# Optimization experiments

Measured on AMD Instinct MI355X. Metric: run time of the kernel, lower is better.

The kernel has to match this reference:

```python
import jax, jax.numpy as jnp
import numpy as np

C = 1.0        # curvature parameter (manifold curvature -1/C)
EPS = 1e-7


def expmap0_space(v, k):
    # v: [..., ds] spatial tangent vector at the hyperboloid origin (time comp 0)
    # returns ambient point [..., ds+1] = (sqrt(k)cosh(|v|/sqrt(k)), sqrt(k)sinh(|v|/sqrt(k)) v/|v|)
    sk = jnp.sqrt(k)
    n = jnp.maximum(jnp.linalg.norm(v, axis=-1, keepdims=True), EPS)
    t = sk * jnp.cosh(n / sk)
    s = sk * jnp.sinh(n / sk) * (v / n)
    return jnp.concatenate([t, s], axis=-1)


def logmap0_space(p, k):
    # p: [..., ds+1] hyperboloid point -> spatial tangent [..., ds] at origin
    sk = jnp.sqrt(k)
    t, s = p[..., :1], p[..., 1:]
    ns = jnp.maximum(jnp.linalg.norm(s, axis=-1, keepdims=True), EPS)
    d = sk * jnp.arccosh(jnp.maximum(t / sk, 1.0 + EPS))
    return d * (s / ns)


def setup_inputs() -> dict:
    key = jax.random.key(0)
    N, DS, E = 50000, 127, 800000
    ks = jax.random.split(key, 8)
    x = jax.random.normal(ks[0], (N, DS), dtype=jnp.float32) * 0.1
    edge_src = jax.random.randint(ks[1], (E,), 0, N)
    edge_dst = jax.random.randint(ks[2], (E,), 0, N)
    edge_weight = jax.random.uniform(ks[3], (E,), dtype=jnp.float32) / 16.0  # ~1/deg norm
    sc = 1.0 / np.sqrt(DS)
    W1 = jax.random.normal(ks[4], (DS, DS), dtype=jnp.float32) * sc
    b1 = jnp.zeros((DS,), dtype=jnp.float32)
    W2 = jax.random.normal(ks[5], (DS, DS), dtype=jnp.float32) * sc
    b2 = jnp.zeros((DS,), dtype=jnp.float32)
    return {"x": x, "W1": W1, "b1": b1, "W2": W2, "b2": b2,
            "edge_src": edge_src, "edge_dst": edge_dst, "edge_weight": edge_weight}


def reference(x, W1, b1, W2, b2, edge_src, edge_dst, edge_weight):
    N = x.shape[0]
    # encode(): cat zero time column + expmap0 onto hyperboloid
    p = expmap0_space(x, C)                 # [N, ds+1]
    h = logmap0_space(p, C)                 # tangent features at origin [N, ds]
    for (W, b) in ((W1, b1), (W2, b2)):
        # hyperbolic linear in tangent space
        z = h @ W + b                       # [N, ds]
        # adjacency-based neighbor aggregation (sparse spmm via edge list)
        msg = edge_weight[:, None] * z[edge_src]          # [E, ds] irregular gather
        agg = jax.ops.segment_sum(msg, edge_dst, num_segments=N)
        # activation + skip connection, back onto the manifold between layers
        h = jax.nn.relu(agg) + h
        h = logmap0_space(expmap0_space(h, C), C)
    return expmap0_space(h, C)              # [N, ds+1] on hyperboloid
```

## Files before the change

kernel.cpp:

```cpp
#include <hip/hip_runtime.h>

#define EPS 1e-7f
#define DS 127
#define DP 128
#define NBMAX 512
#define CAP 4096
#define CH 2048
#define PADB ((DP * DP + DP + 255) / 256)

typedef short bf16x8 __attribute__((ext_vector_type(8)));
typedef float f32x4  __attribute__((ext_vector_type(4)));
typedef float f32x2  __attribute__((ext_vector_type(2)));

__device__ __forceinline__ float wave_sum(float v) {
#pragma unroll
    for (int off = 32; off > 0; off >>= 1)
        v += __shfl_xor(v, off, 64);
    return v;
}

__device__ __forceinline__ int wave_sum_i(int v) {
#pragma unroll
    for (int off = 32; off > 0; off >>= 1)
        v += __shfl_xor(v, off, 64);
    return v;
}

__device__ __forceinline__ unsigned short f2bf(float f) {
    unsigned u = __float_as_uint(f);
    unsigned r = (u + 0x7FFFu + ((u >> 16) & 1u)) >> 16;
    return (unsigned short)r;
}

__device__ __forceinline__ unsigned pack_bf2(float a, float b) {
    return (unsigned)f2bf(a) | ((unsigned)f2bf(b) << 16);
}

__device__ __forceinline__ unsigned char f2fp8(float v) {
    return (unsigned char)(__builtin_amdgcn_cvt_pk_fp8_f32(v, v, 0, false) & 0xFF);
}

__device__ __forceinline__ float logexp_scale(float n2) {
    float nrm = sqrtf(n2);
    return (nrm >= 4.472136e-4f) ? 1.0f : (4.472136e-4f / fmaxf(nrm, EPS));
}

__device__ __forceinline__ void sinhcosh(float n, float& sh, float& ch) {
    float e  = __expf(n);
    float em = __expf(-n);
    sh = 0.5f * (e - em);
    ch = 0.5f * (e + em);
}

__device__ __forceinline__ void padT_dev(int pb, int tid,
        const float* __restrict__ W, const float* __restrict__ b,
        unsigned short* __restrict__ Wt, float* __restrict__ bp) {
    int i = pb * 256 + tid;
    if (i < DP * DP) {
        int n = i >> 7, k = i & (DP - 1);
        Wt[i] = (k < DS && n < DS) ? f2bf(W[k * DS + n]) : (unsigned short)0;
    } else if (i < DP * DP + DP) {
        int j = i - DP * DP;
        bp[j] = (j < DS) ? b[j] : 0.f;
    }
}

__device__ __forceinline__ void f_first_dev(int fbid, int tid,
        const float* __restrict__ x, unsigned* __restrict__ hbu, int N) {
    int gw   = fbid * 4 + (tid >> 6);
    int lane = tid & 63;
    if (gw >= N) return;

    const float* row = x + (size_t)gw * DS;
    float x0 = row[2 * lane];
    float x1 = (lane < 63) ? row[2 * lane + 1] : 0.f;

    float scale = logexp_scale(wave_sum(x0 * x0 + x1 * x1));
    hbu[(size_t)gw * (DP / 2) + lane] = pack_bf2(scale * x0,
                                                 (lane < 63) ? scale * x1 : 0.f);
}

__device__ void binA_dev(int abid, int tid,
        const int* __restrict__ es, const int* __restrict__ ed,
        const float* __restrict__ ew,
        int* __restrict__ gcnt, unsigned* __restrict__ stg_pk,
        unsigned char* __restrict__ stg_r, int E) {
    __shared__ int  lcnt[NBMAX];
    __shared__ int  loff[NBMAX];
    __shared__ int  gbase[NBMAX];
    __shared__ unsigned       lst_pk[CH];
    __shared__ unsigned short lst_d[CH];

    int lane = tid & 63;
    int base = abid * CH;
    int cnt  = min(CH, E - base);

    for (int b = tid; b < NBMAX; b += 256) lcnt[b] = 0;
    __syncthreads();

    unsigned pk[CH / 256];
    int      rd[CH / 256];
#pragma unroll
    for (int k = 0; k < CH / 256; k++) {
        int i = base + k * 256 + tid;
        if (i < E) {
            int d = ed[i];
            rd[k] = d;
            pk[k] = ((unsigned)f2bf(ew[i]) << 16) | (unsigned)es[i];
            atomicAdd(&lcnt[d >> 7], 1);
        } else {
            rd[k] = -1;
        }
    }
    __syncthreads();

    if (tid < 64) {
        int carry = 0;
        for (int c = 0; c < NBMAX; c += 64) {
            int v = lcnt[c + lane];
            int inc = v;
#pragma unroll
            for (int off = 1; off < 64; off <<= 1) {
                int t = __shfl_up(inc, off, 64);
                if (lane >= off) inc += t;
            }
            loff[c + lane] = carry + inc - v;
            carry += __shfl(inc, 63, 64);
        }
    }
    __syncthreads();
    for (int b = tid; b < NBMAX; b += 256) lcnt[b] = 0;
    __syncthreads();

#pragma unroll
    for (int k = 0; k < CH / 256; k++) {
        if (rd[k] >= 0) {
            int b = rd[k] >> 7;
            int slot = loff[b] + atomicAdd(&lcnt[b], 1);
            lst_pk[slot] = pk[k];
            lst_d[slot]  = (unsigned short)rd[k];
        }
    }
    __syncthreads();

    for (int b = tid; b < NBMAX; b += 256) {
        int c = lcnt[b];
        gbase[b] = c ? atomicAdd(&gcnt[b], c) : 0;
    }
    __syncthreads();

    for (int s = tid; s < cnt; s += 256) {
        unsigned p = lst_pk[s];
        int d = lst_d[s];
        int b = d >> 7;
        int idx = gbase[b] + (s - loff[b]);
        if (idx >= CAP) idx = CAP - 1;
        stg_pk[(size_t)b * CAP + idx] = p;
        stg_r [(size_t)b * CAP + idx] = (unsigned char)(d & 127);
    }
}

__global__ __launch_bounds__(256) void mega1(
        const float* __restrict__ x, unsigned* __restrict__ hbu, int N,
        const float* __restrict__ W1, const float* __restrict__ b1,
        unsigned short* __restrict__ Wt1, float* __restrict__ bp1,
        const float* __restrict__ W2, const float* __restrict__ b2,
        unsigned short* __restrict__ Wt2, float* __restrict__ bp2,
        const int* __restrict__ es, const int* __restrict__ ed,
        const float* __restrict__ ew,
        int* __restrict__ gcnt, unsigned* __restrict__ stg_pk,
        unsigned char* __restrict__ stg_r, int E, int nA) {
    int bid = blockIdx.x;
    int tid = threadIdx.x;

    if (bid < nA) {
        binA_dev(bid, tid, es, ed, ew, gcnt, stg_pk, stg_r, E);
        return;
    }
    bid -= nA;

    if (bid < 2 * PADB) {
        int layer = (bid >= PADB);
        int pb    = bid - layer * PADB;
        padT_dev(pb, tid, layer ? W2 : W1, layer ? b2 : b1,
                 layer ? Wt2 : Wt1, layer ? bp2 : bp1);
        return;
    }
    bid -= 2 * PADB;

    f_first_dev(bid, tid, x, hbu, N);
}

__device__ void binB_dev(int b, int tid,
        const unsigned* __restrict__ stg_pk, const unsigned char* __restrict__ stg_r,
        const int* __restrict__ gcnt,
        int* __restrict__ row_start, unsigned* __restrict__ epk,
        int N, int E) {
    __shared__ int rcnt[128];
    __shared__ int roff[128];
    __shared__ int sh_bb;

    int lane = tid & 63;
    int wave = tid >> 6;
    int cnt  = min(gcnt[b], CAP);
    const unsigned*      in_pk = stg_pk + (size_t)b * CAP;
    const unsigned char* in_r  = stg_r  + (size_t)b * CAP;

    if (tid < 128) rcnt[tid] = 0;
    if (b == 0 && tid == 0) row_start[N] = E;
    __syncthreads();

    if (wave == 3) {
        int acc = 0;
        for (int c = lane; c < b; c += 64) acc += min(gcnt[c], CAP);
        acc = wave_sum_i(acc);
        if (lane == 0) sh_bb = acc;
    } else {
        for (int i = tid; i < cnt; i += 192)
            atomicAdd(&rcnt[in_r[i]], 1);
    }
    __syncthreads();
    int bb = sh_bb;

    if (tid < 64) {
        int carry = 0;
        for (int c = 0; c < 128; c += 64) {
            int v = rcnt[c + lane];
            int inc = v;
#pragma unroll
            for (int off = 1; off < 64; off <<= 1) {
                int t = __shfl_up(inc, off, 64);
                if (lane >= off) inc += t;
            }
            roff[c + lane] = carry + inc - v;
            carry += __shfl(inc, 63, 64);
        }
    }
    __syncthreads();

    if (tid < 128) {
        int row = b * 128 + tid;
        if (row < N) row_start[row] = bb + roff[tid];
        rcnt[tid] = 0;
    }
    __syncthreads();

    for (int i = tid; i < cnt; i += 256) {
        int r = in_r[i];
        int pos = atomicAdd(&rcnt[r], 1);
        epk[bb + roff[r] + pos] = in_pk[i];
    }
}

#define BM 64
__device__ void gemm_dev(int gbid, int tid,
        const unsigned short* __restrict__ hb,
        const unsigned short* __restrict__ Wt,
        const float* __restrict__ bp,
        unsigned char* __restrict__ z8, int N) {
    int wave = tid >> 6;
    int lane = tid & 63;
    int m    = lane & 15;
    int quad = lane >> 4;
    int r0   = gbid * BM + wave * 16;

    f32x4 acc[8];
#pragma unroll
    for (int t = 0; t < 8; t++) acc[t] = (f32x4){0.f, 0.f, 0.f, 0.f};

    const bf16x8* arow = (const bf16x8*)(hb + (size_t)(r0 + m) * DP);
#pragma unroll
    for (int kq = 0; kq < 4; kq++) {
        bf16x8 a = arow[kq * 4 + quad];
#pragma unroll
        for (int nt = 0; nt < 8; nt++) {
            bf16x8 bfr = ((const bf16x8*)(Wt + (size_t)(nt * 16 + m) * DP))[kq * 4 + quad];
            acc[nt] = __builtin_amdgcn_mfma_f32_16x16x32_bf16(a, bfr, acc[nt], 0, 0, 0);
        }
    }

#pragma unroll
    for (int nt = 0; nt < 8; nt++) {
        float bias = bp[nt * 16 + m];
#pragma unroll
        for (int reg = 0; reg < 4; reg++) {
            int row = r0 + quad * 4 + reg;
            if (row < N)
                z8[(size_t)row * DP + nt * 16 + m] = f2fp8(acc[nt][reg] + bias);
        }
    }
}

__global__ __launch_bounds__(256) void mega2(
        const unsigned* __restrict__ stg_pk, const unsigned char* __restrict__ stg_r,
        const int* __restrict__ gcnt,
        int* __restrict__ row_start, unsigned* __restrict__ epk,
        const unsigned short* __restrict__ hb,
        const unsigned short* __restrict__ Wt,
        const float* __restrict__ bp,
        unsigned char* __restrict__ z8, int N, int E, int nB) {
    int bid = blockIdx.x;
    int tid = threadIdx.x;
    if (bid < nB) {
        binB_dev(bid, tid, stg_pk, stg_r, gcnt, row_start, epk, N, E);
        return;
    }
    gemm_dev(bid - nB, tid, hb, Wt, bp, z8, N);
}

#define GATHER(K)                                                             \
    {                                                                         \
        unsigned pks[K], us[K];                                               \
        _Pragma("unroll")                                                     \
        for (int i = 0; i < K; i++) pks[i] = epk[e + i];                      \
        _Pragma("unroll")                                                     \
        for (int i = 0; i < K; i++)                                           \
            us[i] = *(const unsigned short*)(zc + (((pks[i] & 0xFFFFu) << 7) + lane2)); \
        _Pragma("unroll")                                                     \
        for (int i = 0; i < K; i++) {                                         \
            float wf = __uint_as_float(pks[i] & 0xFFFF0000u);                 \
            f32x2 zv = __builtin_amdgcn_cvt_pk_f32_fp8(us[i], false);         \
            a0 = fmaf(wf, zv.x, a0);                                          \
            a1 = fmaf(wf, zv.y, a1);                                          \
        }                                                                     \
    }

#define GATHER_TAIL(K)                                                        \
    {                                                                         \
        unsigned pks[K], us[K];                                               \
        _Pragma("unroll")                                                     \
        for (int i = 0; i < K; i++) {                                         \
            int ii = e + i;                                                   \
            int ic = (ii < end) ? ii : (end - 1);                             \
            unsigned p = epk[ic];                                             \
            pks[i] = (ii < end) ? p : 0u;                                     \
        }                                                                     \
        _Pragma("unroll")                                                     \
        for (int i = 0; i < K; i++)                                           \
            us[i] = *(const unsigned short*)(zc + (((pks[i] & 0xFFFFu) << 7) + lane2)); \
        _Pragma("unroll")                                                     \
        for (int i = 0; i < K; i++) {                                         \
            float wf = __uint_as_float(pks[i] & 0xFFFF0000u);                 \
            f32x2 zv = __builtin_amdgcn_cvt_pk_f32_fp8(us[i], false);         \
            a0 = fmaf(wf, zv.x, a0);                                          \
            a1 = fmaf(wf, zv.y, a1);                                          \
        }                                                                     \
    }

template <bool LAST>
__global__ __launch_bounds__(256) void agg_f_tpl(
                          const unsigned char* __restrict__ zc,
                          const unsigned* __restrict__ hbu_in,
                          const int* __restrict__ row_start,
                          const unsigned* __restrict__ epk,
                          unsigned* __restrict__ hbu_out,
                          float* __restrict__ out, int N) {
    int gw   = (int)((blockIdx.x * blockDim.x + threadIdx.x) >> 6);
    int lane = threadIdx.x & 63;
    if (gw >= N) return;
    gw = __builtin_amdgcn_readfirstlane(gw);
    int lane2 = lane << 1;

    int beg = row_start[gw], end = row_start[gw + 1];
    float a0 = 0.f, a1 = 0.f;

    int e = beg;
    for (; e + 16 <= end; e += 16) GATHER(16)
    if (e < end) GATHER_TAIL(16)

    unsigned hu = hbu_in[(size_t)gw * (DP / 2) + lane];
    float x0 = __uint_as_float(hu << 16) + fmaxf(a0, 0.f);
    float x1 = (lane < 63) ? __uint_as_float(hu & 0xFFFF0000u) + fmaxf(a1, 0.f)
                           : 0.f;

    float n2 = wave_sum(x0 * x0 + x1 * x1);
    float scale = logexp_scale(n2);
    float y0 = scale * x0;
    float y1 = (lane < 63) ? scale * x1 : 0.f;

    if (!LAST) {
        hbu_out[(size_t)gw * (DP / 2) + lane] = pack_bf2(y0, y1);
    } else {
        float n2y = scale * scale * n2;
        float ny  = fmaxf(sqrtf(n2y), EPS);
        float shy, chy;
        sinhcosh(ny, shy, chy);
        float sc  = shy / ny;
        float* orow = out + (size_t)gw * DP;
        if (lane == 0) orow[0] = chy;
        orow[1 + 2 * lane] = sc * y0;
        if (lane < 63) orow[2 + 2 * lane] = sc * y1;
    }
}

extern "C" void kernel_launch(void* const* d_in, const int* in_sizes, int n_in,
                              void* d_out, int out_size, void* d_ws, size_t ws_size,
                              hipStream_t stream) {
    const float* x  = (const float*)d_in[0];
    const float* W1 = (const float*)d_in[1];
    const float* b1 = (const float*)d_in[2];
    const float* W2 = (const float*)d_in[3];
    const float* b2 = (const float*)d_in[4];
    const int*   es = (const int*)d_in[5];
    const int*   ed = (const int*)d_in[6];
    const float* ew = (const float*)d_in[7];

    const int N  = in_sizes[0] / DS;
    const int E  = in_sizes[5];
    const int NR = (N + BM - 1) / BM * BM;
    const int NB = (N + 127) >> 7;

    unsigned short* hb  = (unsigned short*)d_ws;
    unsigned char*  z8  = (unsigned char*)(hb + (size_t)NR * DP);
    unsigned short* Wt1 = (unsigned short*)(z8 + (size_t)N * DP);
    unsigned short* Wt2 = Wt1 + DP * DP;
    float* bp1          = (float*)(Wt2 + DP * DP);
    float* bp2          = bp1 + DP;
    unsigned* epk       = (unsigned*)(bp2 + DP);
    int*   row_start    = (int*)(epk + E);
    int*   gcnt         = row_start + N + 1;
    unsigned* stg_pk    = (unsigned*)(gcnt + NBMAX);
    unsigned char* stg_r = (unsigned char*)(stg_pk + (size_t)NBMAX * CAP);

    unsigned* hbu = (unsigned*)hb;

    const int fBlocks    = (N * 64 + 255) / 256;
    const int gemmBlocks = (N + BM - 1) / BM;
    const int binABlocks = (E + CH - 1) / CH;

    hipMemsetAsync(gcnt, 0, NBMAX * sizeof(int), stream);

    mega1<<<binABlocks + 2 * PADB + fBlocks, 256, 0, stream>>>(
        x, hbu, N, W1, b1, Wt1, bp1, W2, b2, Wt2, bp2,
        es, ed, ew, gcnt, stg_pk, stg_r, E, binABlocks);

    mega2<<<NB + gemmBlocks, 256, 0, stream>>>(
        stg_pk, stg_r, gcnt, row_start, epk, hb, Wt1, bp1, z8, N, E, NB);

    agg_f_tpl<false><<<fBlocks, 256, 0, stream>>>(z8, hbu, row_start, epk,
                                                  hbu, nullptr, N);

    mega2<<<gemmBlocks, 256, 0, stream>>>(
        stg_pk, stg_r, gcnt, row_start, epk, hb, Wt2, bp2, z8, N, E, 0);

    agg_f_tpl<true><<<fBlocks, 256, 0, stream>>>(z8, hbu, row_start, epk,
                                                 nullptr, (float*)d_out, N);
}
```

Baseline: 220.0 us.

## Fuse first encode into layer-1 GEMM, process two rows per wave in aggregation

The initial expmap/logmap encode of x moves out of the first mega kernel and into the layer-1 GEMM blocks. Each block normalises its 64 rows, stages them as bf16 in LDS and feeds MFMA directly from there, which removes a global round trip of h before the first GEMM. The aggregation kernel now handles two destination rows per wave, and the row histogram in binB reads uchar4. The second-layer GEMM becomes a standalone kernel. The fused GEMM adds 16 KB of LDS and more register pressure in a kernel that shares blocks with binB, and handling two rows serially per wave may reduce parallelism in the gather.

```diff
diff --git a/kernel.cpp b/kernel.cpp
--- a/kernel.cpp
+++ b/kernel.cpp
@@ -7,6 +7,7 @@
 #define CAP 4096
 #define CH 2048
 #define PADB ((DP * DP + DP + 255) / 256)
+#define BM 64
 
 typedef short bf16x8 __attribute__((ext_vector_type(8)));
 typedef float f32x4  __attribute__((ext_vector_type(4)));
@@ -65,21 +66,6 @@
     }
 }
 
-__device__ __forceinline__ void f_first_dev(int fbid, int tid,
-        const float* __restrict__ x, unsigned* __restrict__ hbu, int N) {
-    int gw   = fbid * 4 + (tid >> 6);
-    int lane = tid & 63;
-    if (gw >= N) return;
-
-    const float* row = x + (size_t)gw * DS;
-    float x0 = row[2 * lane];
-    float x1 = (lane < 63) ? row[2 * lane + 1] : 0.f;
-
-    float scale = logexp_scale(wave_sum(x0 * x0 + x1 * x1));
-    hbu[(size_t)gw * (DP / 2) + lane] = pack_bf2(scale * x0,
-                                                 (lane < 63) ? scale * x1 : 0.f);
-}
-
 __device__ void binA_dev(int abid, int tid,
         const int* __restrict__ es, const int* __restrict__ ed,
         const float* __restrict__ ew,
@@ -160,37 +146,6 @@
     }
 }
 
-__global__ __launch_bounds__(256) void mega1(
-        const float* __restrict__ x, unsigned* __restrict__ hbu, int N,
-        const float* __restrict__ W1, const float* __restrict__ b1,
-        unsigned short* __restrict__ Wt1, float* __restrict__ bp1,
-        const float* __restrict__ W2, const float* __restrict__ b2,
-        unsigned short* __restrict__ Wt2, float* __restrict__ bp2,
-        const int* __restrict__ es, const int* __restrict__ ed,
-        const float* __restrict__ ew,
-        int* __restrict__ gcnt, unsigned* __restrict__ stg_pk,
-        unsigned char* __restrict__ stg_r, int E, int nA) {
-    int bid = blockIdx.x;
-    int tid = threadIdx.x;
-
-    if (bid < nA) {
-        binA_dev(bid, tid, es, ed, ew, gcnt, stg_pk, stg_r, E);
-        return;
-    }
-    bid -= nA;
-
-    if (bid < 2 * PADB) {
-        int layer = (bid >= PADB);
-        int pb    = bid - layer * PADB;
-        padT_dev(pb, tid, layer ? W2 : W1, layer ? b2 : b1,
-                 layer ? Wt2 : Wt1, layer ? bp2 : bp1);
-        return;
-    }
-    bid -= 2 * PADB;
-
-    f_first_dev(bid, tid, x, hbu, N);
-}
-
 __device__ void binB_dev(int b, int tid,
         const unsigned* __restrict__ stg_pk, const unsigned char* __restrict__ stg_r,
         const int* __restrict__ gcnt,
@@ -216,7 +171,16 @@
         acc = wave_sum_i(acc);
         if (lane == 0) sh_bb = acc;
     } else {
-        for (int i = tid; i < cnt; i += 192)
+        int n4 = cnt >> 2;
+        const uchar4* in_r4 = (const uchar4*)in_r;
+        for (int i = tid; i < n4; i += 192) {
+            uchar4 v = in_r4[i];
+            atomicAdd(&rcnt[v.x], 1);
+            atomicAdd(&rcnt[v.y], 1);
+            atomicAdd(&rcnt[v.z], 1);
+            atomicAdd(&rcnt[v.w], 1);
+        }
+        for (int i = (n4 << 2) + tid; i < cnt; i += 192)
             atomicAdd(&rcnt[in_r[i]], 1);
     }
     __syncthreads();
@@ -252,52 +216,101 @@
     }
 }
 
-#define BM 64
-__device__ void gemm_dev(int gbid, int tid,
-        const unsigned short* __restrict__ hb,
-        const unsigned short* __restrict__ Wt,
-        const float* __restrict__ bp,
+__global__ __launch_bounds__(256) void k1_kernel(
+        const int* __restrict__ es, const int* __restrict__ ed,
+        const float* __restrict__ ew,
+        int* __restrict__ gcnt, unsigned* __restrict__ stg_pk,
+        unsigned char* __restrict__ stg_r, int E,
+        const float* __restrict__ W1, const float* __restrict__ b1,
+        unsigned short* __restrict__ Wt1, float* __restrict__ bp1,
+        const float* __restrict__ W2, const float* __restrict__ b2,
+        unsigned short* __restrict__ Wt2, float* __restrict__ bp2, int nA) {
+    int bid = blockIdx.x;
+    int tid = threadIdx.x;
+    if (bid < nA) {
+        binA_dev(bid, tid, es, ed, ew, gcnt, stg_pk, stg_r, E);
+        return;
+    }
+    bid -= nA;
+    int layer = (bid >= PADB);
+    int pb    = bid - layer * PADB;
+    padT_dev(pb, tid, layer ? W2 : W1, layer ? b2 : b1,
+             layer ? Wt2 : Wt1, layer ? bp2 : bp1);
+}
+
+__device__ void fgemm_dev(int gbid, int tid,
+        const float* __restrict__ x, unsigned* __restrict__ hbu,
+        const unsigned short* __restrict__ Wt, const float* __restrict__ bp,
         unsigned char* __restrict__ z8, int N) {
+    __shared__ unsigned sha[64 * 64];
+
     int wave = tid >> 6;
     int lane = tid & 63;
+    int r0   = gbid * BM;
+
+    f32x2 xv[16];
+#pragma unroll
+    for (int r = 0; r < 16; r++) {
+        int row = r0 + wave * 16 + r;
+        if (row < N) {
+            const float* rp = x + (size_t)row * DS;
+            xv[r].x = rp[2 * lane];
+            xv[r].y = (lane < 63) ? rp[2 * lane + 1] : 0.f;
+        } else {
+            xv[r].x = 0.f; xv[r].y = 0.f;
+        }
+    }
+#pragma unroll
+    for (int r = 0; r < 16; r++) {
+        int lr  = wave * 16 + r;
+        int row = r0 + lr;
+        float s = logexp_scale(wave_sum(xv[r].x * xv[r].x + xv[r].y * xv[r].y));
+        unsigned pk = pack_bf2(s * xv[r].x, (lane < 63) ? s * xv[r].y : 0.f);
+        sha[lr * 64 + lane] = pk;
+        if (row < N) hbu[(size_t)row * (DP / 2) + lane] = pk;
+    }
+
     int m    = lane & 15;
     int quad = lane >> 4;
-    int r0   = gbid * BM + wave * 16;
 
     f32x4 acc[8];
 #pragma unroll
     for (int t = 0; t < 8; t++) acc[t] = (f32x4){0.f, 0.f, 0.f, 0.f};
 
-    const bf16x8* arow = (const bf16x8*)(hb + (size_t)(r0 + m) * DP);
+    const unsigned* shrow = sha + (size_t)(wave * 16 + m) * 64;
+    bf16x8 a[4];
+#pragma unroll
+    for (int kq = 0; kq < 4; kq++)
+        a[kq] = *(const bf16x8*)(shrow + kq * 16 + quad * 4);
+
 #pragma unroll
     for (int kq = 0; kq < 4; kq++) {
-        bf16x8 a = arow[kq * 4 + quad];
 #pragma unroll
         for (int nt = 0; nt < 8; nt++) {
             bf16x8 bfr = ((const bf16x8*)(Wt + (size_t)(nt * 16 + m) * DP))[kq * 4 + quad];
-            acc[nt] = __builtin_amdgcn_mfma_f32_16x16x32_bf16(a, bfr, acc[nt], 0, 0, 0);
-        }
-    }
-
+            acc[nt] = __builtin_amdgcn_mfma_f32_16x16x32_bf16(a[kq], bfr, acc[nt], 0, 0, 0);
+        }
+    }
+
+    int rw0 = r0 + wave * 16;
 #pragma unroll
     for (int nt = 0; nt < 8; nt++) {
         float bias = bp[nt * 16 + m];
 #pragma unroll
         for (int reg = 0; reg < 4; reg++) {
-            int row = r0 + quad * 4 + reg;
+            int row = rw0 + quad * 4 + reg;
             if (row < N)
                 z8[(size_t)row * DP + nt * 16 + m] = f2fp8(acc[nt][reg] + bias);
         }
     }
 }
 
-__global__ __launch_bounds__(256) void mega2(
+__global__ __launch_bounds__(256) void k2_kernel(
         const unsigned* __restrict__ stg_pk, const unsigned char* __restrict__ stg_r,
         const int* __restrict__ gcnt,
         int* __restrict__ row_start, unsigned* __restrict__ epk,
-        const unsigned short* __restrict__ hb,
-        const unsigned short* __restrict__ Wt,
-        const float* __restrict__ bp,
+        const float* __restrict__ x, unsigned* __restrict__ hbu,
+        const unsigned short* __restrict__ Wt, const float* __restrict__ bp,
         unsigned char* __restrict__ z8, int N, int E, int nB) {
     int bid = blockIdx.x;
     int tid = threadIdx.x;
@@ -305,47 +318,90 @@
         binB_dev(bid, tid, stg_pk, stg_r, gcnt, row_start, epk, N, E);
         return;
     }
-    gemm_dev(bid - nB, tid, hb, Wt, bp, z8, N);
-}
-
-#define GATHER(K)                                                             \
-    {                                                                         \
-        unsigned pks[K], us[K];                                               \
-        _Pragma("unroll")                                                     \
-        for (int i = 0; i < K; i++) pks[i] = epk[e + i];                      \
-        _Pragma("unroll")                                                     \
-        for (int i = 0; i < K; i++)                                           \
-            us[i] = *(const unsigned short*)(zc + (((pks[i] & 0xFFFFu) << 7) + lane2)); \
-        _Pragma("unroll")                                                     \
-        for (int i = 0; i < K; i++) {                                         \
-            float wf = __uint_as_float(pks[i] & 0xFFFF0000u);                 \
-            f32x2 zv = __builtin_amdgcn_cvt_pk_f32_fp8(us[i], false);         \
-            a0 = fmaf(wf, zv.x, a0);                                          \
-            a1 = fmaf(wf, zv.y, a1);                                          \
-        }                                                                     \
-    }
-
-#define GATHER_TAIL(K)                                                        \
-    {                                                                         \
-        unsigned pks[K], us[K];                                               \
-        _Pragma("unroll")                                                     \
-        for (int i = 0; i < K; i++) {                                         \
-            int ii = e + i;                                                   \
-            int ic = (ii < end) ? ii : (end - 1);                             \
-            unsigned p = epk[ic];                                             \
-            pks[i] = (ii < end) ? p : 0u;                                     \
-        }                                                                     \
-        _Pragma("unroll")                                                     \
-        for (int i = 0; i < K; i++)                                           \
-            us[i] = *(const unsigned short*)(zc + (((pks[i] & 0xFFFFu) << 7) + lane2)); \
-        _Pragma("unroll")                                                     \
-        for (int i = 0; i < K; i++) {                                         \
-            float wf = __uint_as_float(pks[i] & 0xFFFF0000u);                 \
-            f32x2 zv = __builtin_amdgcn_cvt_pk_f32_fp8(us[i], false);         \
-            a0 = fmaf(wf, zv.x, a0);                                          \
-            a1 = fmaf(wf, zv.y, a1);                                          \
-        }                                                                     \
-    }
+    fgemm_dev(bid - nB, tid, x, hbu, Wt, bp, z8, N);
+}
+
+__global__ __launch_bounds__(256) void gemm_kernel(
+        const unsigned short* __restrict__ hb,
+        const unsigned short* __restrict__ Wt,
+        const float* __restrict__ bp,
+        unsigned char* __restrict__ z8, int N) {
+    int wave = threadIdx.x >> 6;
+    int lane = threadIdx.x & 63;
+    int m    = lane & 15;
+    int quad = lane >> 4;
+    int r0   = blockIdx.x * BM + wave * 16;
+
+    f32x4 acc[8];
+#pragma unroll
+    for (int t = 0; t < 8; t++) acc[t] = (f32x4){0.f, 0.f, 0.f, 0.f};
+
+    const bf16x8* arow = (const bf16x8*)(hb + (size_t)(r0 + m) * DP);
+    bf16x8 a[4];
+#pragma unroll
+    for (int kq = 0; kq < 4; kq++) a[kq] = arow[kq * 4 + quad];
+
+#pragma unroll
+    for (int kq = 0; kq < 4; kq++) {
+#pragma unroll
+        for (int nt = 0; nt < 8; nt++) {
+            bf16x8 bfr = ((const bf16x8*)(Wt + (size_t)(nt * 16 + m) * DP))[kq * 4 + quad];
+            acc[nt] = __builtin_amdgcn_mfma_f32_16x16x32_bf16(a[kq], bfr, acc[nt], 0, 0, 0);
+        }
+    }
+
+#pragma unroll
+    for (int nt = 0; nt < 8; nt++) {
+        float bias = bp[nt * 16 + m];
+#pragma unroll
+        for (int reg = 0; reg < 4; reg++) {
+            int row = r0 + quad * 4 + reg;
+            if (row < N)
+                z8[(size_t)row * DP + nt * 16 + m] = f2fp8(acc[nt][reg] + bias);
+        }
+    }
+}
+
+__device__ __forceinline__ void gather16(const unsigned char* __restrict__ zc,
+        const unsigned* __restrict__ epk, int e, int lane2,
+        float& a0, float& a1) {
+    unsigned pks[16], us[16];
+#pragma unroll
+    for (int i = 0; i < 16; i++) pks[i] = epk[e + i];
+#pragma unroll
+    for (int i = 0; i < 16; i++)
+        us[i] = *(const unsigned short*)(zc + (((pks[i] & 0xFFFFu) << 7) + lane2));
+#pragma unroll
+    for (int i = 0; i < 16; i++) {
+        float wf = __uint_as_float(pks[i] & 0xFFFF0000u);
+        f32x2 zv = __builtin_amdgcn_cvt_pk_f32_fp8(us[i], false);
+        a0 = fmaf(wf, zv.x, a0);
+        a1 = fmaf(wf, zv.y, a1);
+    }
+}
+
+__device__ __forceinline__ void gather_tail16(const unsigned char* __restrict__ zc,
+        const unsigned* __restrict__ epk, int e, int end, int lane2,
+        float& a0, float& a1) {
+    unsigned pks[16], us[16];
+#pragma unroll
+    for (int i = 0; i < 16; i++) {
+        int ii = e + i;
+        int ic = (ii < end) ? ii : (end - 1);
+        unsigned p = epk[ic];
+        pks[i] = (ii < end) ? p : 0u;
+    }
+#pragma unroll
+    for (int i = 0; i < 16; i++)
+        us[i] = *(const unsigned short*)(zc + (((pks[i] & 0xFFFFu) << 7) + lane2));
+#pragma unroll
+    for (int i = 0; i < 16; i++) {
+        float wf = __uint_as_float(pks[i] & 0xFFFF0000u);
+        f32x2 zv = __builtin_amdgcn_cvt_pk_f32_fp8(us[i], false);
+        a0 = fmaf(wf, zv.x, a0);
+        a1 = fmaf(wf, zv.y, a1);
+    }
+}
 
 template <bool LAST>
 __global__ __launch_bounds__(256) void agg_f_tpl(
@@ -355,41 +411,58 @@
                           const unsigned* __restrict__ epk,
                           unsigned* __restrict__ hbu_out,
                           float* __restrict__ out, int N) {
-    int gw   = (int)((blockIdx.x * blockDim.x + threadIdx.x) >> 6);
+    int wid  = (int)((blockIdx.x * blockDim.x + threadIdx.x) >> 6);
     int lane = threadIdx.x & 63;
-    if (gw >= N) return;
-    gw = __builtin_amdgcn_readfirstlane(gw);
+    int gw0  = wid * 2;
+    if (gw0 >= N) return;
+    gw0 = __builtin_amdgcn_readfirstlane(gw0);
     int lane2 = lane << 1;
-
-    int beg = row_start[gw], end = row_start[gw + 1];
-    float a0 = 0.f, a1 = 0.f;
-
-    int e = beg;
-    for (; e + 16 <= end; e += 16) GATHER(16)
-    if (e < end) GATHER_TAIL(16)
-
-    unsigned hu = hbu_in[(size_t)gw * (DP / 2) + lane];
-    float x0 = __uint_as_float(hu << 16) + fmaxf(a0, 0.f);
-    float x1 = (lane < 63) ? __uint_as_float(hu & 0xFFFF0000u) + fmaxf(a1, 0.f)
-                           : 0.f;
-
-    float n2 = wave_sum(x0 * x0 + x1 * x1);
-    float scale = logexp_scale(n2);
-    float y0 = scale * x0;
-    float y1 = (lane < 63) ? scale * x1 : 0.f;
-
-    if (!LAST) {
-        hbu_out[(size_t)gw * (DP / 2) + lane] = pack_bf2(y0, y1);
-    } else {
-        float n2y = scale * scale * n2;
-        float ny  = fmaxf(sqrtf(n2y), EPS);
-        float shy, chy;
-        sinhcosh(ny, shy, chy);
-        float sc  = shy / ny;
-        float* orow = out + (size_t)gw * DP;
-        if (lane == 0) orow[0] = chy;
-        orow[1 + 2 * lane] = sc * y0;
-        if (lane < 63) orow[2 + 2 * lane] = sc * y1;
+    bool has1 = (gw0 + 1 < N);
+
+    int rs0 = row_start[gw0];
+    int rs1 = row_start[gw0 + 1];
+    int rs2 = has1 ? row_start[gw0 + 2] : rs1;
+    unsigned hu0 = hbu_in[(size_t)gw0 * (DP / 2) + lane];
+    unsigned hu1 = has1 ? hbu_in[(size_t)(gw0 + 1) * (DP / 2) + lane] : 0u;
+
+    int begs[2] = {rs0, rs1};
+    int ends[2] = {rs1, rs2};
+    float a0[2] = {0.f, 0.f}, a1[2] = {0.f, 0.f};
+
+#pragma unroll
+    for (int r = 0; r < 2; r++) {
+        int e = begs[r], end = ends[r];
+        for (; e + 16 <= end; e += 16) gather16(zc, epk, e, lane2, a0[r], a1[r]);
+        if (e < end) gather_tail16(zc, epk, e, end, lane2, a0[r], a1[r]);
+    }
+
+    unsigned hus[2] = {hu0, hu1};
+#pragma unroll
+    for (int r = 0; r < 2; r++) {
+        if (r == 1 && !has1) break;
+        int gw = gw0 + r;
+        float x0 = __uint_as_float(hus[r] << 16) + fmaxf(a0[r], 0.f);
+        float x1 = (lane < 63) ? __uint_as_float(hus[r] & 0xFFFF0000u) + fmaxf(a1[r], 0.f)
+                               : 0.f;
+
+        float n2 = wave_sum(x0 * x0 + x1 * x1);
+        float scale = logexp_scale(n2);
+        float y0 = scale * x0;
+        float y1 = (lane < 63) ? scale * x1 : 0.f;
+
+        if (!LAST) {
+            hbu_out[(size_t)gw * (DP / 2) + lane] = pack_bf2(y0, y1);
+        } else {
+            float n2y = scale * scale * n2;
+            float ny  = fmaxf(sqrtf(n2y), EPS);
+            float shy, chy;
+            sinhcosh(ny, shy, chy);
+            float sc  = shy / ny;
+            float* orow = out + (size_t)gw * DP;
+            if (lane == 0) orow[0] = chy;
+            orow[1 + 2 * lane] = sc * y0;
+            if (lane < 63) orow[2 + 2 * lane] = sc * y1;
+        }
     }
 }
 
@@ -424,25 +497,26 @@
 
     unsigned* hbu = (unsigned*)hb;
 
-    const int fBlocks    = (N * 64 + 255) / 256;
     const int gemmBlocks = (N + BM - 1) / BM;
     const int binABlocks = (E + CH - 1) / CH;
+    const int aggWaves   = (N + 1) / 2;
+    const int aggBlocks  = (aggWaves + 3) / 4;
 
     hipMemsetAsync(gcnt, 0, NBMAX * sizeof(int), stream);
 
-    mega1<<<binABlocks + 2 * PADB + fBlocks, 256, 0, stream>>>(
-        x, hbu, N, W1, b1, Wt1, bp1, W2, b2, Wt2, bp2,
-        es, ed, ew, gcnt, stg_pk, stg_r, E, binABlocks);
-
-    mega2<<<NB + gemmBlocks, 256, 0, stream>>>(
-        stg_pk, stg_r, gcnt, row_start, epk, hb, Wt1, bp1, z8, N, E, NB);
-
-    agg_f_tpl<false><<<fBlocks, 256, 0, stream>>>(z8, hbu, row_start, epk,
-                                                  hbu, nullptr, N);
-
-    mega2<<<gemmBlocks, 256, 0, stream>>>(
-        stg_pk, stg_r, gcnt, row_start, epk, hb, Wt2, bp2, z8, N, E, 0);
-
-    agg_f_tpl<true><<<fBlocks, 256, 0, stream>>>(z8, hbu, row_start, epk,
-                                                 nullptr, (float*)d_out, N);
-}
+    k1_kernel<<<binABlocks + 2 * PADB, 256, 0, stream>>>(
+        es, ed, ew, gcnt, stg_pk, stg_r, E,
+        W1, b1, Wt1, bp1, W2, b2, Wt2, bp2, binABlocks);
+
+    k2_kernel<<<NB + gemmBlocks, 256, 0, stream>>>(
+        stg_pk, stg_r, gcnt, row_start, epk,
+        x, hbu, Wt1, bp1, z8, N, E, NB);
+
+    agg_f_tpl<false><<<aggBlocks, 256, 0, stream>>>(z8, hbu, row_start, epk,
+                                                    hbu, nullptr, N);
+
+    gemm_kernel<<<gemmBlocks, 256, 0, stream>>>(hb, Wt2, bp2, z8, N);
+
+    agg_f_tpl<true><<<aggBlocks, 256, 0, stream>>>(z8, hbu, row_start, epk,
+                                                   nullptr, (float*)d_out, N);
+}
```

Measured after the change: 223.2 us. Within noise of the previous version (+1.5%).
